# Kernel tuning notes

Hardware: AMD Instinct MI355X
Metric: run time of the kernel (lower is better)

Reference implementation:

```python
import jax, jax.numpy as jnp
import numpy as np

TEXT_DIM = 1024
FEAT_DIM = 1024
NUM_HEADS = 16
HEAD_DIM = FEAT_DIM // NUM_HEADS
EPS = 1e-6


def rms_norm(x, w):
    # LlamaRMSNorm: compute in fp32, scale by learned weight
    xf = x.astype(jnp.float32)
    var = jnp.mean(xf * xf, axis=-1, keepdims=True)
    return (xf * jax.lax.rsqrt(var + EPS)).astype(x.dtype) * w


def setup_inputs() -> dict:
    key = jax.random.key(0)
    ks = jax.random.split(key, 8)
    def xavier(k, shape, gain=1.0):
        fan_in, fan_out = shape[1], shape[0]
        lim = gain * np.sqrt(6.0 / (fan_in + fan_out))
        return jax.random.uniform(k, shape, jnp.float32, -lim, lim)
    return {
        "text": jax.random.normal(ks[0], (8, 512, TEXT_DIM), jnp.float32),
        "features": jax.random.normal(ks[1], (8, 1024, FEAT_DIM), jnp.float32),
        "W_q": xavier(ks[2], (FEAT_DIM, TEXT_DIM)),
        "b_q": jnp.zeros((FEAT_DIM,), jnp.float32),
        "W_k": xavier(ks[3], (FEAT_DIM, FEAT_DIM)),
        "b_k": jnp.zeros((FEAT_DIM,), jnp.float32),
        "W_o": xavier(ks[4], (FEAT_DIM, FEAT_DIM), gain=0.1),
        "b_o": jnp.zeros((FEAT_DIM,), jnp.float32),
        "g_feat": jnp.ones((FEAT_DIM,), jnp.float32),
        "g_q": jnp.ones((FEAT_DIM,), jnp.float32),
        "g_k": jnp.ones((FEAT_DIM,), jnp.float32),
    }


def reference(text, features, W_q, b_q, W_k, b_k, W_o, b_o, g_feat, g_q, g_k):
    B, T, _ = text.shape
    _, N, _ = features.shape
    feats = rms_norm(features, g_feat)                      # [B,N,Df]
    Q = rms_norm(text @ W_q.T + b_q, g_q)                   # [B,T,Df]
    K = rms_norm(feats @ W_k.T + b_k, g_k)                  # [B,N,Df]
    Qh = Q.reshape(B, T, NUM_HEADS, HEAD_DIM)
    Kh = K.reshape(B, N, NUM_HEADS, HEAD_DIM)
    Vh = feats.reshape(B, N, NUM_HEADS, HEAD_DIM)
    scores = jnp.einsum("bthd,bnhd->bhtn", Qh, Kh) / np.sqrt(HEAD_DIM).astype(np.float32)
    attn = jax.nn.softmax(scores, axis=-1)                  # [B,H,T,N]
    out = jnp.einsum("bhtn,bnhd->bthd", attn, Vh).reshape(B, T, FEAT_DIM)
    return out @ W_o.T + b_o
```

## Files before the change

### kernel.cpp

```cpp
#include <hip/hip_runtime.h>
#include <hip/hip_bf16.h>


typedef unsigned short u16;
typedef __bf16 bf16x8 __attribute__((ext_vector_type(8)));
typedef float f32x4 __attribute__((ext_vector_type(4)));

extern "C" __device__ float __ocml_native_exp2_f32(float);

__device__ inline f32x4 mfma16(bf16x8 a, bf16x8 b, f32x4 c) {
    return __builtin_amdgcn_mfma_f32_16x16x32_bf16(a, b, c, 0, 0, 0);
}

__device__ inline u16 f2bf(float f) {
    union { float f; unsigned u; } v; v.f = f;
    unsigned r = v.u + 0x7fffu + ((v.u >> 16) & 1u);
    return (u16)(r >> 16);
}

__device__ inline unsigned pk_bf16(float a, float b) {
    union { float f; unsigned u; } x, y; x.f = a; y.f = b;
    return __builtin_amdgcn_perm(y.u + 0x8000u, x.u + 0x8000u, 0x07060302u);
}

__device__ inline unsigned cvt_pk(float a, float b) {
    unsigned r;
    asm("v_cvt_pk_bf16_f32 %0, %1, %2" : "=v"(r) : "v"(a), "v"(b));
    return r;
}

__device__ inline void load_lds16(const void* g, void* l) {
    __builtin_amdgcn_global_load_lds(
        (const __attribute__((address_space(1))) void*)g,
        (__attribute__((address_space(3))) void*)l, 16, 0, 0);
}

__global__ __launch_bounds__(256) void cast_rows_kernel(const float* __restrict__ text,
                                                        const float* __restrict__ Wq,
                                                        const float* __restrict__ Wk,
                                                        const float* __restrict__ Wo,
                                                        const float* __restrict__ features,
                                                        const float* __restrict__ g_feat,
                                                        u16* __restrict__ otext, u16* __restrict__ oWq,
                                                        u16* __restrict__ oWk, u16* __restrict__ oWo,
                                                        u16* __restrict__ feats_bf,
                                                        float* __restrict__ qkss) {
    int blk = blockIdx.x, tid = threadIdx.x;
    if (blk < 7168) {
        int i = blk * 256 + tid;
        const float* src; u16* dst; int off;
        if (i < 1048576)      { src = text; dst = otext; off = i; }
        else if (i < 1310720) { src = Wq;   dst = oWq;   off = i - 1048576; }
        else if (i < 1572864) { src = Wk;   dst = oWk;   off = i - 1310720; }
        else                  { src = Wo;   dst = oWo;   off = i - 1572864; }
        float4 v = ((const float4*)src)[off];
        uint2 p; p.x = pk_bf16(v.x, v.y); p.y = pk_bf16(v.z, v.w);
        ((uint2*)dst)[off] = p;
    } else {
        int i2 = (blk - 7168) * 256 + tid;
        if (i2 < 12288) qkss[i2] = 0.0f;
        int row = (blk - 7168) * 4 + (tid >> 6);
        int lane = tid & 63;
        const float4* rp = (const float4*)(features + (size_t)row * 1024) + lane * 4;
        float4 v[4];
        float ss = 0.0f;
        #pragma unroll
        for (int i = 0; i < 4; ++i) {
            v[i] = rp[i];
            ss += v[i].x * v[i].x + v[i].y * v[i].y + v[i].z * v[i].z + v[i].w * v[i].w;
        }
        #pragma unroll
        for (int m = 1; m < 64; m <<= 1) ss += __shfl_xor(ss, m, 64);
        float rs = rsqrtf(ss * (1.0f / 1024.0f) + 1e-6f);
        const float4* gp = (const float4*)(g_feat) + lane * 4;
        union { unsigned u[8]; uint4 q[2]; } ob;
        #pragma unroll
        for (int i = 0; i < 4; ++i) {
            float4 gv = gp[i];
            ob.u[i * 2]     = pk_bf16(v[i].x * rs * gv.x, v[i].y * rs * gv.y);
            ob.u[i * 2 + 1] = pk_bf16(v[i].z * rs * gv.z, v[i].w * rs * gv.w);
        }
        uint4* dst = (uint4*)(feats_bf + (size_t)row * 1024 + lane * 16);
        dst[0] = ob.q[0];
        dst[1] = ob.q[1];
    }
}

template <bool BF16OUT, bool NORM>
__device__ __forceinline__ void gemm64_bk64(const u16* __restrict__ A, const u16* __restrict__ B,
                                            const float* __restrict__ bias,
                                            const float* __restrict__ gvec,
                                            float* __restrict__ ssout,
                                            void* __restrict__ Cout,
                                            int m_blk, int n_blk, int K, int N,
                                            u16* As, u16* Bs) {
    int tid = threadIdx.x, wave = tid >> 6, lane = tid & 63;
    int quad = lane >> 4, l15 = lane & 15;
    int wm = wave & 1, wn = wave >> 1;
    int srl = lane >> 3, scl = lane & 7;
    const int swz = (scl ^ srl) * 8;

    f32x4 acc[4][2] = {};

    auto stage = [&](int buf, int k0) {
        u16* Ad = As + buf * (128 * 64);
        u16* Bd = Bs + buf * (64 * 64);
        #pragma unroll
        for (int is = 0; is < 4; ++is) {
            int row = is * 32 + wave * 8 + srl;
            load_lds16(A + (size_t)(m_blk + row) * K + k0 + swz,
                       Ad + (is * 32 + wave * 8) * 64);
        }
        #pragma unroll
        for (int is = 0; is < 2; ++is) {
            int row = is * 32 + wave * 8 + srl;
            load_lds16(B + (size_t)(n_blk + row) * K + k0 + swz,
                       Bd + (is * 32 + wave * 8) * 64);
        }
    };

    stage(0, 0);
    __syncthreads();
    int cur = 0;

    for (int k0 = 0; k0 < K; k0 += 64) {
        if (k0 + 64 < K) stage(cur ^ 1, k0 + 64);

        const u16* Ar = As + cur * (128 * 64);
        const u16* Br = Bs + cur * (64 * 64);
        #pragma unroll
        for (int kh = 0; kh < 2; ++kh) {
            bf16x8 af[4], bfr[2];
            int co = ((kh * 4 + quad) ^ (l15 & 7)) * 8;
            #pragma unroll
            for (int t = 0; t < 4; ++t)
                af[t] = *(const bf16x8*)&Ar[(wm * 64 + t * 16 + l15) * 64 + co];
            #pragma unroll
            for (int t = 0; t < 2; ++t)
                bfr[t] = *(const bf16x8*)&Br[(wn * 32 + t * 16 + l15) * 64 + co];
            #pragma unroll
            for (int mt = 0; mt < 4; ++mt)
                #pragma unroll
                for (int nt = 0; nt < 2; ++nt)
                    acc[mt][nt] = mfma16(af[mt], bfr[nt], acc[mt][nt]);
        }
        __syncthreads();
        cur ^= 1;
    }

    float bv[2], gv[2];
    #pragma unroll
    for (int nt = 0; nt < 2; ++nt) {
        int col = n_blk + wn * 32 + nt * 16 + l15;
        bv[nt] = bias[col];
        if (NORM) gv[nt] = gvec[col];
    }
    #pragma unroll
    for (int mt = 0; mt < 4; ++mt) {
        int row0 = m_blk + wm * 64 + mt * 16 + quad * 4;
        #pragma unroll
        for (int nt = 0; nt < 2; ++nt)
            #pragma unroll
            for (int r = 0; r < 4; ++r)
                acc[mt][nt][r] += bv[nt];
        if (NORM) {
            f32x4 ss4 = {0.0f, 0.0f, 0.0f, 0.0f};
            #pragma unroll
            for (int nt = 0; nt < 2; ++nt)
                #pragma unroll
                for (int r = 0; r < 4; ++r)
                    ss4[r] += acc[mt][nt][r] * acc[mt][nt][r];
            #pragma unroll
            for (int m = 1; m < 16; m <<= 1)
                #pragma unroll
                for (int r = 0; r < 4; ++r)
                    ss4[r] += __shfl_xor(ss4[r], m, 64);
            if (l15 == 0) {
                #pragma unroll
                for (int r = 0; r < 4; ++r)
                    atomicAdd(&ssout[row0 + r], ss4[r]);
            }
        }
        #pragma unroll
        for (int nt = 0; nt < 2; ++nt) {
            int col = n_blk + wn * 32 + nt * 16 + l15;
            #pragma unroll
            for (int r = 0; r < 4; ++r) {
                float val = NORM ? acc[mt][nt][r] * gv[nt] : acc[mt][nt][r];
                if (BF16OUT) ((u16*)Cout)[(size_t)(row0 + r) * N + col] = f2bf(val);
                else       ((float*)Cout)[(size_t)(row0 + r) * N + col] = val;
            }
        }
    }
}

__global__ __launch_bounds__(256) void gemm_qk_kernel(const u16* __restrict__ text_bf,
                                                      const u16* __restrict__ Wq,
                                                      const u16* __restrict__ feats_bf,
                                                      const u16* __restrict__ Wk,
                                                      const float* __restrict__ b_q,
                                                      const float* __restrict__ b_k,
                                                      const float* __restrict__ g_q,
                                                      const float* __restrict__ g_k,
                                                      float* __restrict__ qkss,
                                                      u16* __restrict__ QK,
                                                      u16* __restrict__ Vt) {
    __shared__ __align__(16) u16 As[2 * 128 * 64];
    __shared__ __align__(16) u16 Bs[2 * 64 * 64];
    int id = blockIdx.x;
    if (id < 512) {
        gemm64_bk64<true, true>(text_bf, Wq, b_q, g_q, qkss, QK,
                                (id & 31) * 128, (id >> 5) * 64, 1024, 1024, As, Bs);
    } else if (id < 1536) {
        id -= 512;
        gemm64_bk64<true, true>(feats_bf, Wk, b_k, g_k, qkss + 4096, QK + 4096 * 1024,
                                (id & 63) * 128, (id >> 6) * 64, 1024, 1024, As, Bs);
    } else {
        id -= 1536;
        int n0 = (id & 15) * 64, d0 = ((id >> 4) & 15) * 64, b = id >> 8;
        u16 (*tile)[72] = (u16(*)[72])As;
        int tid = threadIdx.x;
        int r = tid >> 2, cs = (tid & 3) * 16;
        int grow = b * 1024 + n0 + r;

        const uint4* src = (const uint4*)(feats_bf + (size_t)grow * 1024 + d0 + cs);
        union { u16 s[16]; uint4 v[2]; } ob;
        ob.v[0] = src[0];
        ob.v[1] = src[1];
        #pragma unroll
        for (int i = 0; i < 16; ++i) tile[r][cs + i] = ob.s[i];
        __syncthreads();
        union { u16 s[8]; uint4 v; } t0, t1;
        #pragma unroll
        for (int i = 0; i < 8; ++i) { t0.s[i] = tile[cs + i][r]; t1.s[i] = tile[cs + 8 + i][r]; }
        u16* tdst = Vt + ((size_t)(b * 1024 + d0 + r)) * 1024 + n0 + cs;
        *(uint4*)tdst = t0.v;
        *(uint4*)(tdst + 8) = t1.v;
    }
}

__global__ __launch_bounds__(256) void gemm_o_kernel(const u16* __restrict__ A,
                                                     const u16* __restrict__ B,
                                                     const float* __restrict__ bias,
                                                     float* __restrict__ C) {
    __shared__ __align__(16) u16 As[2 * 128 * 64];
    __shared__ __align__(16) u16 Bs[2 * 64 * 64];
    int id = blockIdx.x;
    gemm64_bk64<false, false>(A, B, bias, nullptr, nullptr, C,
                              (id & 31) * 128, (id >> 5) * 64, 1024, 1024, As, Bs);
}

__global__ __launch_bounds__(256, 4) void attn_kernel(const u16* __restrict__ Q,
                                                      const u16* __restrict__ K,
                                                      const u16* __restrict__ Vt,
                                                      const float* __restrict__ qkss,
                                                      u16* __restrict__ Out) {
    const float QSCALE = 0.18033688011112042f;
    int bh = blockIdx.x, qt = blockIdx.y;
    int b = bh >> 4, h = bh & 15;
    int tid = threadIdx.x, wave = tid >> 6, lane = tid & 63;
    int quad = lane >> 4, l15 = lane & 15;
    int wq = wave & 1, wn = wave >> 1;

    __shared__ __align__(16) u16 Ks[2][64 * 64];
    __shared__ __align__(16) u16 Vs[2][64 * 64];
    __shared__ __align__(16) u16 Plds[4][2 * 16 * 32];
    u16* Pw = &Plds[wave][0];
    const int pfs = (l15 >> 1) & 3;

    bf16x8 qf[2][2];
    float rsq[2];
    #pragma unroll
    for (int mt = 0; mt < 2; ++mt) {
        int qrow = b * 512 + qt * 64 + wq * 32 + mt * 16 + l15;
        const size_t qoff = (size_t)qrow * 1024 + h * 64 + quad * 8;
        qf[mt][0] = *(const bf16x8*)(Q + qoff);
        qf[mt][1] = *(const bf16x8*)(Q + qoff + 32);
        rsq[mt] = rsqrtf(qkss[qrow] * (1.0f / 1024.0f) + 1e-6f) * QSCALE;
    }
    const float* ssk = qkss + 4096 + b * 1024;

    int srl = lane >> 3, scl = lane & 7;
    const u16* Kbase = K + ((size_t)(b * 1024)) * 1024 + h * 64;
    const u16* Vbase = Vt + ((size_t)(b * 1024 + h * 64)) * 1024;

    __bf16 onev = (__bf16)1.0f;
    bf16x8 ones = {onev, onev, onev, onev, onev, onev, onev, onev};

    f32x4 o[2][4] = {};
    f32x4 lac[2] = {{0.0f, 0.0f, 0.0f, 0.0f}, {0.0f, 0.0f, 0.0f, 0.0f}};

    auto stage = [&](int buf, int n0) {
        #pragma unroll
        for (int j = 0; j < 2; ++j) {
            int row = wave * 16 + j * 8 + srl;
            load_lds16(Kbase + (size_t)(n0 + row) * 1024 + (scl ^ srl) * 8,
                       &Ks[buf][(wave * 16 + j * 8) * 64]);
            load_lds16(Vbase + (size_t)row * 1024 + n0 + (scl ^ srl) * 8,
                       &Vs[buf][(wave * 16 + j * 8) * 64]);
        }
    };

    stage(0, 0);
    __syncthreads();
    int cur = 0;

    for (int n0 = 0; n0 < 1024; n0 += 64) {
        if (n0 < 960) stage(cur ^ 1, n0 + 64);

        f32x4 s[2][2];
        __builtin_amdgcn_s_setprio(1);
        #pragma unroll
        for (int nt = 0; nt < 2; ++nt) {
            int R = wn * 32 + nt * 16 + l15;
            int c1 = (quad ^ (l15 & 7)) * 8;
            bf16x8 kf0 = *(const bf16x8*)&Ks[cur][R * 64 + c1];
            bf16x8 kf1 = *(const bf16x8*)&Ks[cur][R * 64 + (c1 ^ 32)];
            #pragma unroll
            for (int mt = 0; mt < 2; ++mt) {
                f32x4 z = {0.0f, 0.0f, 0.0f, 0.0f};
                s[mt][nt] = mfma16(kf0, qf[mt][0], z);
                s[mt][nt] = mfma16(kf1, qf[mt][1], s[mt][nt]);
            }
        }
        __builtin_amdgcn_s_setprio(0);

        #pragma unroll
        for (int nt = 0; nt < 2; ++nt) {
            int nb = n0 + wn * 32 + nt * 16 + quad * 4;
            f32x4 kss = *(const f32x4*)&ssk[nb];
            f32x4 rsn;
            #pragma unroll
            for (int r = 0; r < 4; ++r)
                rsn[r] = rsqrtf(kss[r] * (1.0f / 1024.0f) + 1e-6f);
            #pragma unroll
            for (int mt = 0; mt < 2; ++mt) {
                float e[4];
                #pragma unroll
                for (int r = 0; r < 4; ++r)
                    e[r] = __ocml_native_exp2_f32(fmaf(s[mt][nt][r], rsn[r] * rsq[mt], -16.0f));
                uint2 pk;
                pk.x = cvt_pk(e[0], e[1]);
                pk.y = cvt_pk(e[2], e[3]);
                *(uint2*)&Pw[mt * 512 + l15 * 32 + (((nt * 4 + quad) ^ (pfs << 1)) << 2)] = pk;
            }
        }

        bf16x8 pf[2], vf[4];
        #pragma unroll
        for (int mt = 0; mt < 2; ++mt)
            pf[mt] = *(const bf16x8*)&Pw[mt * 512 + l15 * 32 + ((quad ^ pfs) << 3)];
        #pragma unroll
        for (int dt = 0; dt < 4; ++dt) {
            int ch = ((wn * 4 + quad) ^ (l15 & 7)) * 8;
            vf[dt] = *(const bf16x8*)&Vs[cur][(dt * 16 + l15) * 64 + ch];
        }
        __builtin_amdgcn_s_setprio(1);
        #pragma unroll
        for (int mt = 0; mt < 2; ++mt) {
            lac[mt] = mfma16(ones, pf[mt], lac[mt]);
            #pragma unroll
            for (int dt = 0; dt < 4; ++dt)
                o[mt][dt] = mfma16(vf[dt], pf[mt], o[mt][dt]);
        }
        __builtin_amdgcn_s_setprio(0);

        __syncthreads();
        cur ^= 1;
    }

    float* Ored = (float*)&Ks[0][0];
    float* Lred = (float*)&Vs[0][0];
    if (wn == 1) {
        #pragma unroll
        for (int mt = 0; mt < 2; ++mt) {
            #pragma unroll
            for (int dt = 0; dt < 4; ++dt) {
                int c = mt * 4 + dt;
                *(f32x4*)&Ored[wq * 2048 + lane * 32 + ((c ^ (lane & 7)) << 2)] = o[mt][dt];
            }
            Lred[wq * 128 + lane * 2 + mt] = lac[mt][0];
        }
    }
    __syncthreads();
    if (wn == 0) {
        #pragma unroll
        for (int mt = 0; mt < 2; ++mt) {
            float il = 1.0f / (lac[mt][0] + Lred[wq * 128 + lane * 2 + mt]);
            size_t obase =
                ((size_t)(b * 512 + qt * 64 + wq * 32 + mt * 16 + l15)) * 1024 + h * 64 + quad * 4;
            #pragma unroll
            for (int dt = 0; dt < 4; ++dt) {
                int c = mt * 4 + dt;
                f32x4 oo = o[mt][dt] + *(const f32x4*)&Ored[wq * 2048 + lane * 32 + ((c ^ (lane & 7)) << 2)];
                uint2 pk;
                pk.x = cvt_pk(oo[0] * il, oo[1] * il);
                pk.y = cvt_pk(oo[2] * il, oo[3] * il);
                *(uint2*)(Out + obase + dt * 16) = pk;
            }
        }
    }
}

extern "C" void kernel_launch(void* const* d_in, const int* in_sizes, int n_in,
                              void* d_out, int out_size, void* d_ws, size_t ws_size,
                              hipStream_t stream) {
    const float* text     = (const float*)d_in[0];
    const float* features = (const float*)d_in[1];
    const float* W_q      = (const float*)d_in[2];
    const float* b_q      = (const float*)d_in[3];
    const float* W_k      = (const float*)d_in[4];
    const float* b_k      = (const float*)d_in[5];
    const float* W_o      = (const float*)d_in[6];
    const float* b_o      = (const float*)d_in[7];
    const float* g_feat   = (const float*)d_in[8];
    const float* g_q      = (const float*)d_in[9];
    const float* g_k      = (const float*)d_in[10];

    char* ws = (char*)d_ws;
    u16*   text_bf  = (u16*)(ws + 0);
    u16*   Wq_bf    = (u16*)(ws + 8388608);
    u16*   Wk_bf    = (u16*)(ws + 10485760);
    u16*   Wo_bf    = (u16*)(ws + 12582912);
    u16*   feats_bf = (u16*)(ws + 14680064);
    u16*   Vt       = (u16*)(ws + 31457280);
    u16*   QKbuf    = (u16*)(ws + 48234496);
    u16*   attn_bf  = (u16*)(ws + 73400320);
    float* qkss     = (float*)(ws + 81821696);

    cast_rows_kernel<<<9216, 256, 0, stream>>>(text, W_q, W_k, W_o, features, g_feat,
                                               text_bf, Wq_bf, Wk_bf, Wo_bf,
                                               feats_bf, qkss);
    gemm_qk_kernel<<<3584, 256, 0, stream>>>(text_bf, Wq_bf, feats_bf, Wk_bf,
                                             b_q, b_k, g_q, g_k, qkss, QKbuf, Vt);
    attn_kernel<<<dim3(128, 8), 256, 0, stream>>>(QKbuf, QKbuf + 4096 * 1024, Vt, qkss, attn_bf);
    gemm_o_kernel<<<512, 256, 0, stream>>>(attn_bf, Wo_bf, b_o, (float*)d_out);
}
```

Baseline: 212.8 us.

## Double attention query tile per block to share K/V staging across eight waves

The attention kernel now handles 128 query rows per block with 512 threads (eight waves) instead of 64 rows with four waves. Each wave stages one 8-row slice of the shared K/V tile, so every K/V tile pulled into LDS serves twice as many queries. Shared memory becomes a single flat buffer, and the final cross-wave reduction scratch is remapped into it. The trade-off is half as many blocks in the grid and a larger LDS footprint per block, which may lower occupancy and reduce latency hiding.

```diff
diff --git a/kernel.cpp b/kernel.cpp
--- a/kernel.cpp
+++ b/kernel.cpp
@@ -250,29 +250,30 @@
                               (id & 31) * 128, (id >> 5) * 64, 1024, 1024, As, Bs);
 }
 
-__global__ __launch_bounds__(256, 4) void attn_kernel(const u16* __restrict__ Q,
-                                                      const u16* __restrict__ K,
-                                                      const u16* __restrict__ Vt,
-                                                      const float* __restrict__ qkss,
-                                                      u16* __restrict__ Out) {
+__global__ __launch_bounds__(512) void attn_kernel(const u16* __restrict__ Q,
+                                                   const u16* __restrict__ K,
+                                                   const u16* __restrict__ Vt,
+                                                   const float* __restrict__ qkss,
+                                                   u16* __restrict__ Out) {
     const float QSCALE = 0.18033688011112042f;
     int bh = blockIdx.x, qt = blockIdx.y;
     int b = bh >> 4, h = bh & 15;
     int tid = threadIdx.x, wave = tid >> 6, lane = tid & 63;
     int quad = lane >> 4, l15 = lane & 15;
-    int wq = wave & 1, wn = wave >> 1;
-
-    __shared__ __align__(16) u16 Ks[2][64 * 64];
-    __shared__ __align__(16) u16 Vs[2][64 * 64];
-    __shared__ __align__(16) u16 Plds[4][2 * 16 * 32];
-    u16* Pw = &Plds[wave][0];
+    int wq = wave >> 1, wn = wave & 1;
+
+    __shared__ __align__(16) char smem[49152];
+    u16* Ks = (u16*)smem;
+    u16* Vs = Ks + 8192;
+    u16* Plds = Vs + 8192;
+    u16* Pw = Plds + wave * 1024;
     const int pfs = (l15 >> 1) & 3;
 
     bf16x8 qf[2][2];
     float rsq[2];
     #pragma unroll
     for (int mt = 0; mt < 2; ++mt) {
-        int qrow = b * 512 + qt * 64 + wq * 32 + mt * 16 + l15;
+        int qrow = b * 512 + qt * 128 + wq * 32 + mt * 16 + l15;
         const size_t qoff = (size_t)qrow * 1024 + h * 64 + quad * 8;
         qf[mt][0] = *(const bf16x8*)(Q + qoff);
         qf[mt][1] = *(const bf16x8*)(Q + qoff + 32);
@@ -291,14 +292,11 @@
     f32x4 lac[2] = {{0.0f, 0.0f, 0.0f, 0.0f}, {0.0f, 0.0f, 0.0f, 0.0f}};
 
     auto stage = [&](int buf, int n0) {
-        #pragma unroll
-        for (int j = 0; j < 2; ++j) {
-            int row = wave * 16 + j * 8 + srl;
-            load_lds16(Kbase + (size_t)(n0 + row) * 1024 + (scl ^ srl) * 8,
-                       &Ks[buf][(wave * 16 + j * 8) * 64]);
-            load_lds16(Vbase + (size_t)row * 1024 + n0 + (scl ^ srl) * 8,
-                       &Vs[buf][(wave * 16 + j * 8) * 64]);
-        }
+        int row = wave * 8 + srl;
+        load_lds16(Kbase + (size_t)(n0 + row) * 1024 + (scl ^ srl) * 8,
+                   Ks + buf * 4096 + (wave * 8) * 64);
+        load_lds16(Vbase + (size_t)row * 1024 + n0 + (scl ^ srl) * 8,
+                   Vs + buf * 4096 + (wave * 8) * 64);
     };
 
     stage(0, 0);
@@ -314,8 +312,8 @@
         for (int nt = 0; nt < 2; ++nt) {
             int R = wn * 32 + nt * 16 + l15;
             int c1 = (quad ^ (l15 & 7)) * 8;
-            bf16x8 kf0 = *(const bf16x8*)&Ks[cur][R * 64 + c1];
-            bf16x8 kf1 = *(const bf16x8*)&Ks[cur][R * 64 + (c1 ^ 32)];
+            bf16x8 kf0 = *(const bf16x8*)&Ks[cur * 4096 + R * 64 + c1];
+            bf16x8 kf1 = *(const bf16x8*)&Ks[cur * 4096 + R * 64 + (c1 ^ 32)];
             #pragma unroll
             for (int mt = 0; mt < 2; ++mt) {
                 f32x4 z = {0.0f, 0.0f, 0.0f, 0.0f};
@@ -353,7 +351,7 @@
         #pragma unroll
         for (int dt = 0; dt < 4; ++dt) {
             int ch = ((wn * 4 + quad) ^ (l15 & 7)) * 8;
-            vf[dt] = *(const bf16x8*)&Vs[cur][(dt * 16 + l15) * 64 + ch];
+            vf[dt] = *(const bf16x8*)&Vs[cur * 4096 + (dt * 16 + l15) * 64 + ch];
         }
         __builtin_amdgcn_s_setprio(1);
         #pragma unroll
@@ -369,8 +367,8 @@
         cur ^= 1;
     }
 
-    float* Ored = (float*)&Ks[0][0];
-    float* Lred = (float*)&Vs[0][0];
+    float* Ored = (float*)smem;
+    float* Lred = (float*)(smem + 32768);
     if (wn == 1) {
         #pragma unroll
         for (int mt = 0; mt < 2; ++mt) {
@@ -388,7 +386,7 @@
         for (int mt = 0; mt < 2; ++mt) {
             float il = 1.0f / (lac[mt][0] + Lred[wq * 128 + lane * 2 + mt]);
             size_t obase =
-                ((size_t)(b * 512 + qt * 64 + wq * 32 + mt * 16 + l15)) * 1024 + h * 64 + quad * 4;
+                ((size_t)(b * 512 + qt * 128 + wq * 32 + mt * 16 + l15)) * 1024 + h * 64 + quad * 4;
             #pragma unroll
             for (int dt = 0; dt < 4; ++dt) {
                 int c = mt * 4 + dt;
@@ -433,6 +431,6 @@
                                                feats_bf, qkss);
     gemm_qk_kernel<<<3584, 256, 0, stream>>>(text_bf, Wq_bf, feats_bf, Wk_bf,
                                              b_q, b_k, g_q, g_k, qkss, QKbuf, Vt);
-    attn_kernel<<<dim3(128, 8), 256, 0, stream>>>(QKbuf, QKbuf + 4096 * 1024, Vt, qkss, attn_bf);
+    attn_kernel<<<dim3(128, 4), 512, 0, stream>>>(QKbuf, QKbuf + 4096 * 1024, Vt, qkss, attn_bf);
     gemm_o_kernel<<<512, 256, 0, stream>>>(attn_bf, Wo_bf, b_o, (float*)d_out);
 }
```

New measurement: 210.7 us (median of 2 runs). Within noise of the previous version (-1.0%).
